# Performance work log

Hardware: AMD Instinct MI355X
Metric: run time of the kernel (lower is better)

## Reference

```python
import jax, jax.numpy as jnp
import numpy as np

EMBED_DIM = 1024
NUM_HEADS = 16
HEAD_DIM = EMBED_DIM // NUM_HEADS
BATCH = 1
SEQ = 4096


def setup_inputs() -> dict:
    key = jax.random.key(0)
    ks = jax.random.split(key, 9)
    s = 1.0 / np.sqrt(EMBED_DIM)
    inp = {
        "x": jax.random.normal(ks[0], (BATCH, SEQ, EMBED_DIM), dtype=jnp.float32),
        "Wq": jax.random.uniform(ks[1], (EMBED_DIM, EMBED_DIM), jnp.float32, -s, s),
        "bq": jax.random.uniform(ks[2], (EMBED_DIM,), jnp.float32, -s, s),
        "Wk": jax.random.uniform(ks[3], (EMBED_DIM, EMBED_DIM), jnp.float32, -s, s),
        "bk": jax.random.uniform(ks[4], (EMBED_DIM,), jnp.float32, -s, s),
        "Wv": jax.random.uniform(ks[5], (EMBED_DIM, EMBED_DIM), jnp.float32, -s, s),
        "bv": jax.random.uniform(ks[6], (EMBED_DIM,), jnp.float32, -s, s),
        "Wo": jax.random.uniform(ks[7], (EMBED_DIM, EMBED_DIM), jnp.float32, -s, s),
        "bo": jax.random.uniform(ks[8], (EMBED_DIM,), jnp.float32, -s, s),
    }
    return inp


def _attention(x, Wq, bq, Wk, bk, Wv, bv, Wo, bo):
    B, S, E = x.shape
    # project and split heads: [B, H, S, D]
    def split_heads(t):
        return t.reshape(B, S, NUM_HEADS, HEAD_DIM).transpose(0, 2, 1, 3)
    q = split_heads(x @ Wq + bq)
    k = split_heads(x @ Wk + bk)
    v = split_heads(x @ Wv + bv)
    scale = 1.0 / np.sqrt(HEAD_DIM).astype(np.float32)
    # scores: [B, H, S, S] (torch code materializes these per query chunk;
    # math is identical computed in one shot)
    scores = jnp.einsum("bhqd,bhkd->bhqk", q, k) * scale
    attn = jax.nn.softmax(scores, axis=-1)  # dropout p=0 -> identity
    out = jnp.einsum("bhqk,bhkd->bhqd", attn, v)
    out = out.transpose(0, 2, 1, 3).reshape(B, S, E)
    return out @ Wo + bo


def reference(x, Wq, bq, Wk, bk, Wv, bv, Wo, bo):
    return _attention(x, Wq, bq, Wk, bk, Wv, bv, Wo, bo)
```

## Files before the change

### kernel.cpp

```cpp
#include <hip/hip_runtime.h>
#include <stdint.h>

typedef __bf16 bf16;
typedef __bf16 bf16x2 __attribute__((ext_vector_type(2)));
typedef __bf16 bf16x8 __attribute__((ext_vector_type(8)));
typedef float f32x4 __attribute__((ext_vector_type(4)));
typedef float f32x16 __attribute__((ext_vector_type(16)));
typedef uint32_t u32x2 __attribute__((ext_vector_type(2)));

#define EMB 1024
#define SEQ 4096
#define NH 16
#define HD 64

__device__ __forceinline__ void glds16(const void* g, void* l) {
    __builtin_amdgcn_global_load_lds(
        (const __attribute__((address_space(1))) uint32_t*)(uintptr_t)g,
        (__attribute__((address_space(3))) uint32_t*)(uintptr_t)l,
        16, 0, 0);
}

union PU { bf16x2 h; uint32_t u; };
__device__ __forceinline__ uint32_t pack_bf16(float a, float b) {
    PU p; p.h = (bf16x2){(bf16)a, (bf16)b}; return p.u;
}
union FU { bf16x8 v; uint32_t u[4]; };

template<int NT>
__device__ __forceinline__ void transpose_tile(const float* in, bf16* out,
                                               int R, int C, int rbase, int cbase,
                                               bf16* tile ) {
    const int t = threadIdx.x;
    constexpr int PASSES = 512 / NT;
#pragma unroll
    for (int p = 0; p < PASSES; ++p) {
        int idx = t + p * NT;
        int r = idx >> 3;
        int seg = idx & 7;
        const float* src = in + (size_t)(rbase + r) * C + cbase + seg * 8;
        f32x4 a = *(const f32x4*)src;
        f32x4 b = *(const f32x4*)(src + 4);
#pragma unroll
        for (int i = 0; i < 4; ++i) {
            tile[r * 81 + seg * 8 + i]     = (bf16)a[i];
            tile[r * 81 + seg * 8 + 4 + i] = (bf16)b[i];
        }
    }
    __syncthreads();
#pragma unroll
    for (int p = 0; p < PASSES; ++p) {
        int idx = t + p * NT;
        int r = idx >> 3;
        int seg = idx & 7;
        bf16x8 v;
#pragma unroll
        for (int i = 0; i < 8; ++i) v[i] = tile[(seg * 8 + i) * 81 + r];
        *(bf16x8*)(out + (size_t)(cbase + r) * R + rbase + seg * 8) = v;
    }
}

__global__ __launch_bounds__(256) void prep_k(const float* __restrict__ W0,
                                              const float* __restrict__ W1,
                                              const float* __restrict__ W2,
                                              bf16* __restrict__ o0,
                                              bf16* __restrict__ o1,
                                              bf16* __restrict__ o2,
                                              const float* __restrict__ x,
                                              bf16* __restrict__ xb) {
    __shared__ bf16 tile[64 * 81];
    if (blockIdx.z < 3) {
        const float* in = blockIdx.z == 0 ? W0 : (blockIdx.z == 1 ? W1 : W2);
        bf16* out = blockIdx.z == 0 ? o0 : (blockIdx.z == 1 ? o1 : o2);
        transpose_tile<256>(in, out, EMB, EMB, blockIdx.y * 64, blockIdx.x * 64, tile);
    } else {
        size_t linear = blockIdx.y * 16 + blockIdx.x;
#pragma unroll
        for (int i = 0; i < 4; ++i) {
            size_t base = linear * 16384 + (size_t)i * 4096 + threadIdx.x * 16;
#pragma unroll
            for (int h = 0; h < 2; ++h) {
                f32x4 a = *(const f32x4*)(x + base + h * 8);
                f32x4 b = *(const f32x4*)(x + base + h * 8 + 4);
                bf16x8 v;
#pragma unroll
                for (int j = 0; j < 4; ++j) { v[j] = (bf16)a[j]; v[4 + j] = (bf16)b[j]; }
                *(bf16x8*)(xb + base + h * 8) = v;
            }
        }
    }
}

__global__ __launch_bounds__(256) void transpose_k(const float* __restrict__ in,
                                                   bf16* __restrict__ out,
                                                   int R, int C) {
    __shared__ bf16 tile[64 * 81];
    transpose_tile<256>(in, out, R, C, blockIdx.y * 64, blockIdx.x * 64, tile);
}

template<bool A_BF16, bool FUSED>
__global__ __launch_bounds__(256, 3) void gemm_m97(
    const void* __restrict__ A,
    const bf16* __restrict__ Wt0, const bf16* __restrict__ Wt1,
    const bf16* __restrict__ Wt2,
    const float* __restrict__ b0, const float* __restrict__ b1,
    const float* __restrict__ b2,
    void* __restrict__ out0, void* __restrict__ out1,
    bf16* __restrict__ outVt) {
    constexpr int SMEM_BYTES = A_BF16 ? (FUSED ? 18432 : 16384) : 24576;
    __shared__ __align__(16) uint8_t smem[SMEM_BYTES];
    float* aF = (float*)smem;
    bf16*  aB = (bf16*)smem;
    bf16*  bL = (bf16*)(smem + (A_BF16 ? 8192 : 16384));

    const int t = threadIdx.x;
    const int lane = t & 63;
    const int wave = t >> 6;
    const int l15 = lane & 15;
    const int quad = lane >> 4;
    const int wrow = (wave >> 1) * 64;
    const int wcol = (wave & 1) * 64;
    const int nb = blockIdx.x;
    const int which = FUSED ? (nb >> 3) : 0;
    const int ncol = (FUSED ? (nb & 7) : nb) * 128;
    const int mblock = blockIdx.y * 128;

    const bf16* Wt = FUSED ? (which == 0 ? Wt0 : (which == 1 ? Wt1 : Wt2)) : Wt0;
    const float* bias = FUSED ? (which == 0 ? b0 : (which == 1 ? b1 : b2)) : b0;

    float bv[4];
#pragma unroll
    for (int nt = 0; nt < 4; ++nt) bv[nt] = bias[ncol + wcol + nt * 16 + l15];

    f32x4 acc[4][4];
#pragma unroll
    for (int mt = 0; mt < 4; ++mt)
#pragma unroll
        for (int nt = 0; nt < 4; ++nt) acc[mt][nt] = (f32x4){0.f, 0.f, 0.f, 0.f};

    const int a4row = lane >> 3, a4seg = lane & 7;
    const int b2row = lane >> 2, b2seg = lane & 3;

    for (int k0 = 0; k0 < EMB; k0 += 32) {
        __syncthreads();
        if constexpr (!A_BF16) {
#pragma unroll
            for (int i = 0; i < 4; ++i) {
                int row = i * 32 + wave * 8 + a4row;
                int sg = a4seg ^ (row & 7);
                glds16((const float*)A + (size_t)(mblock + row) * EMB + k0 + sg * 4,
                       smem + i * 4096 + wave * 1024);
            }
        } else {
#pragma unroll
            for (int i = 0; i < 2; ++i) {
                int row = i * 64 + wave * 16 + b2row;
                int sg = b2seg ^ ((row >> 1) & 3);
                glds16((const bf16*)A + (size_t)(mblock + row) * EMB + k0 + sg * 8,
                       smem + i * 4096 + wave * 1024);
            }
        }
#pragma unroll
        for (int i = 0; i < 2; ++i) {
            int row = i * 64 + wave * 16 + b2row;
            int sg = b2seg ^ ((row >> 1) & 3);
            glds16(Wt + (size_t)(ncol + row) * EMB + k0 + sg * 8,
                   (uint8_t*)bL + i * 4096 + wave * 1024);
        }
        __syncthreads();

        bf16x8 af[4], bfr[4];
#pragma unroll
        for (int mt = 0; mt < 4; ++mt) {
            int rl = wrow + mt * 16 + l15;
            if constexpr (!A_BF16) {
                f32x4 lo = *(const f32x4*)(aF + rl * 32 + ((2 * quad)     ^ (rl & 7)) * 4);
                f32x4 hi = *(const f32x4*)(aF + rl * 32 + ((2 * quad + 1) ^ (rl & 7)) * 4);
#pragma unroll
                for (int j = 0; j < 4; ++j) {
                    af[mt][j]     = (bf16)lo[j];
                    af[mt][4 + j] = (bf16)hi[j];
                }
            } else {
                af[mt] = *(const bf16x8*)(aB + rl * 32 + (quad ^ ((rl >> 1) & 3)) * 8);
            }
        }
#pragma unroll
        for (int nt = 0; nt < 4; ++nt) {
            int rl = wcol + nt * 16 + l15;
            bfr[nt] = *(const bf16x8*)(bL + rl * 32 + (quad ^ ((rl >> 1) & 3)) * 8);
        }
#pragma unroll
        for (int mt = 0; mt < 4; ++mt)
#pragma unroll
            for (int nt = 0; nt < 4; ++nt)
                acc[mt][nt] = __builtin_amdgcn_mfma_f32_16x16x32_bf16(
                    af[mt], bfr[nt], acc[mt][nt], 0, 0, 0);
    }

    if (!FUSED || which < 2) {
        void* outp = FUSED ? (which == 0 ? out0 : out1) : out0;
#pragma unroll
        for (int mt = 0; mt < 4; ++mt)
#pragma unroll
            for (int nt = 0; nt < 4; ++nt)
#pragma unroll
                for (int r = 0; r < 4; ++r) {
                    size_t row = mblock + wrow + mt * 16 + quad * 4 + r;
                    size_t col = ncol + wcol + nt * 16 + l15;
                    float v = acc[mt][nt][r] + bv[nt];
                    if constexpr (FUSED) ((bf16*)outp)[row * EMB + col] = (bf16)v;
                    else                 ((float*)outp)[row * EMB + col] = v;
                }
    } else if constexpr (FUSED) {
        __syncthreads();
        bf16* tr = (bf16*)smem + wave * 2304;
#pragma unroll
        for (int ch = 0; ch < 2; ++ch) {
#pragma unroll
            for (int mt = 0; mt < 4; ++mt)
#pragma unroll
                for (int ntl = 0; ntl < 2; ++ntl)
#pragma unroll
                    for (int r = 0; r < 4; ++r) {
                        int d_local = ntl * 16 + l15;
                        int s_local = mt * 16 + quad * 4 + r;
                        int nt = 2 * ch + ntl;
                        tr[d_local * 72 + s_local] = (bf16)(acc[mt][nt][r] + bv[nt]);
                    }
            int d2 = lane & 31, h2 = lane >> 5;
#pragma unroll
            for (int j = 0; j < 4; ++j) {
                bf16x8 v = *(const bf16x8*)(tr + d2 * 72 + h2 * 32 + j * 8);
                *(bf16x8*)(outVt + (size_t)(ncol + wcol + ch * 32 + d2) * SEQ +
                           mblock + wrow + h2 * 32 + j * 8) = v;
            }
        }
    }
}

__global__ __launch_bounds__(256, 2) void attn_k(bf16* __restrict__ QO,
                                                 const bf16* __restrict__ Km,
                                                 const bf16* __restrict__ Vt,
                                                 const float* __restrict__ Wo,
                                                 bf16* __restrict__ wt_o) {
    __shared__ bf16 k_lds[2][64 * 64];
    __shared__ bf16 v_lds[2][64 * 64];

    const int t = threadIdx.x;
    const int lane = t & 63;
    const int wave = t >> 6;
    const int l31 = lane & 31;
    const int hi = lane >> 5;
    const int l7 = lane & 7;
    const int head = blockIdx.y;
    const int qbase = blockIdx.x * 128 + wave * 32;
    const float QSCALE = 0.125f * 1.4426950408889634f;

    const int srow = wave * 16 + (lane >> 3);
    const int ssg  = lane & 7;

    bf16x8 qf[4];
#pragma unroll
    for (int s = 0; s < 4; ++s) {
        bf16x8 raw = *(const bf16x8*)(QO + (size_t)(qbase + l31) * EMB +
                                      head * HD + s * 16 + hi * 8);
#pragma unroll
        for (int j = 0; j < 8; ++j) qf[s][j] = (bf16)((float)raw[j] * QSCALE);
    }

    f32x16 o_acc[2];
#pragma unroll
    for (int db = 0; db < 2; ++db)
#pragma unroll
        for (int z = 0; z < 16; ++z) o_acc[db][z] = 0.f;
    float l_run = 0.f;

#define STAGE(buf, kbv)                                                               \
    do {                                                                              \
        _Pragma("unroll")                                                             \
        for (int i = 0; i < 2; ++i) {                                                 \
            int rr = srow + i * 8;                                                    \
            int sg = ssg ^ (rr & 7);                                                  \
            glds16(Km + (size_t)((kbv) + rr) * EMB + head * HD + sg * 8,              \
                   &k_lds[buf][(wave * 16 + i * 8) * 64]);                            \
            glds16(Vt + (size_t)(head * HD + rr) * SEQ + (kbv) + sg * 8,              \
                   &v_lds[buf][(wave * 16 + i * 8) * 64]);                            \
        }                                                                             \
    } while (0)

#define COMPUTE(buf)                                                                  \
    do {                                                                              \
        f32x16 sa[2];                                                                 \
        _Pragma("unroll")                                                             \
        for (int b = 0; b < 2; ++b)                                                   \
            _Pragma("unroll")                                                         \
            for (int z = 0; z < 16; ++z) sa[b][z] = 0.f;                              \
        __builtin_amdgcn_s_setprio(1);                                                \
        _Pragma("unroll")                                                             \
        for (int s = 0; s < 4; ++s) {                                                 \
            bf16x8 kf0 = *(const bf16x8*)&k_lds[buf][(l31) * 64 +                     \
                            (((2 * s + hi) ^ l7) * 8)];                               \
            bf16x8 kf1 = *(const bf16x8*)&k_lds[buf][(32 + l31) * 64 +                \
                            (((2 * s + hi) ^ l7) * 8)];                               \
            sa[0] = __builtin_amdgcn_mfma_f32_32x32x16_bf16(kf0, qf[s], sa[0], 0, 0, 0);\
            sa[1] = __builtin_amdgcn_mfma_f32_32x32x16_bf16(kf1, qf[s], sa[1], 0, 0, 0);\
        }                                                                             \
        __builtin_amdgcn_s_setprio(0);                                                \
        uint32_t u0[2][4], u1[2][4];                                                  \
        _Pragma("unroll")                                                             \
        for (int b = 0; b < 2; ++b)                                                   \
            _Pragma("unroll")                                                         \
            for (int i = 0; i < 4; ++i) {                                             \
                float p0 = __builtin_amdgcn_exp2f(sa[b][4 * i + 0]);                  \
                float p1 = __builtin_amdgcn_exp2f(sa[b][4 * i + 1]);                  \
                float p2 = __builtin_amdgcn_exp2f(sa[b][4 * i + 2]);                  \
                float p3 = __builtin_amdgcn_exp2f(sa[b][4 * i + 3]);                  \
                l_run += (p0 + p1) + (p2 + p3);                                       \
                u0[b][i] = pack_bf16(p0, p1);                                         \
                u1[b][i] = pack_bf16(p2, p3);                                         \
            }                                                                         \
        __builtin_amdgcn_s_setprio(1);                                                \
        _Pragma("unroll")                                                             \
        for (int tt = 0; tt < 4; ++tt) {                                              \
            const int b = tt >> 1, sp = tt & 1;                                       \
            u32x2 ra = __builtin_amdgcn_permlane32_swap(                              \
                u0[b][2 * sp], u0[b][2 * sp + 1], false, false);                      \
            u32x2 rb = __builtin_amdgcn_permlane32_swap(                              \
                u1[b][2 * sp], u1[b][2 * sp + 1], false, false);                      \
            FU A;                                                                     \
            A.u[0] = ra[0]; A.u[1] = rb[0]; A.u[2] = ra[1]; A.u[3] = rb[1];           \
            bf16x8 vf0 = *(const bf16x8*)&v_lds[buf][(l31) * 64 +                     \
                            (((2 * tt + hi) ^ l7) * 8)];                              \
            bf16x8 vf1 = *(const bf16x8*)&v_lds[buf][(32 + l31) * 64 +                \
                            (((2 * tt + hi) ^ l7) * 8)];                              \
            o_acc[0] = __builtin_amdgcn_mfma_f32_32x32x16_bf16(A.v, vf0, o_acc[0], 0, 0, 0);\
            o_acc[1] = __builtin_amdgcn_mfma_f32_32x32x16_bf16(A.v, vf1, o_acc[1], 0, 0, 0);\
        }                                                                             \
        __builtin_amdgcn_s_setprio(0);                                                \
    } while (0)

    STAGE(0, 0);
    for (int kb = 0; kb < SEQ; kb += 128) {
        __syncthreads();
        STAGE(1, kb + 64);
        COMPUTE(0);
        __syncthreads();
        if (kb + 128 < SEQ) STAGE(0, kb + 128);
        COMPUTE(1);
    }
#undef STAGE
#undef COMPUTE

    l_run += __shfl_xor(l_run, 32);
    float inv = 1.0f / l_run;
    float invr[16];
#pragma unroll
    for (int reg = 0; reg < 16; ++reg)
        invr[reg] = __shfl(inv, (reg & 3) + 8 * (reg >> 2) + 4 * hi);
#pragma unroll
    for (int db = 0; db < 2; ++db)
#pragma unroll
        for (int reg = 0; reg < 16; ++reg) {
            int q = (reg & 3) + 8 * (reg >> 2) + 4 * hi;
            QO[(size_t)(qbase + q) * EMB + head * HD + db * 32 + l31] =
                (bf16)(o_acc[db][reg] * invr[reg]);
        }

    if (Wo != nullptr) {
        int bid = blockIdx.y * gridDim.x + blockIdx.x;
        if (bid < 256) {
            __syncthreads();
            bf16* tile = &k_lds[0][0];
            int ty = bid >> 4, tx = bid & 15;
            transpose_tile<256>(Wo, wt_o, EMB, EMB, ty * 64, tx * 64, tile);
        }
    }
}

extern "C" void kernel_launch(void* const* d_in, const int* in_sizes, int n_in,
                              void* d_out, int out_size, void* d_ws, size_t ws_size,
                              hipStream_t stream) {
    const float* x  = (const float*)d_in[0];
    const float* Wq = (const float*)d_in[1];
    const float* bq = (const float*)d_in[2];
    const float* Wk = (const float*)d_in[3];
    const float* bk = (const float*)d_in[4];
    const float* Wv = (const float*)d_in[5];
    const float* bv = (const float*)d_in[6];
    const float* Wo = (const float*)d_in[7];
    const float* bo = (const float*)d_in[8];

    const size_t MAT = (size_t)SEQ * EMB;
    const size_t WMT = (size_t)EMB * EMB;

    bf16* o16   = (bf16*)d_out;
    bf16* Wt_q  = o16;
    bf16* Wt_k  = o16 + WMT;
    bf16* Wt_v  = o16 + 2 * WMT;
    bf16* Vtb   = o16 + 3 * WMT;

    bf16* wsb   = (bf16*)d_ws;
    bf16* QOb   = wsb;
    bf16* Kb    = wsb + MAT;
    bf16* xb    = wsb + 2 * MAT;

    dim3 blk(256);
    dim3 gP(16, 16, 4);
    dim3 gF(24, SEQ / 128);
    dim3 gO(EMB / 128, SEQ / 128);

    if (ws_size >= 3 * MAT * sizeof(bf16)) {
        prep_k<<<gP, blk, 0, stream>>>(Wq, Wk, Wv, Wt_q, Wt_k, Wt_v, x, xb);

        gemm_m97<true, true><<<gF, blk, 0, stream>>>(
            xb, Wt_q, Wt_k, Wt_v, bq, bk, bv, QOb, Kb, Vtb);

        dim3 gA(SEQ / 128, NH);
        attn_k<<<gA, blk, 0, stream>>>(QOb, Kb, Vtb, Wo, xb);

        gemm_m97<true, false><<<gO, blk, 0, stream>>>(
            QOb, xb, nullptr, nullptr, bo, nullptr, nullptr, d_out, nullptr, nullptr);
    } else {
        bf16* Wt_o = wsb + MAT;
        dim3 gTW(EMB / 64, EMB / 64);
        transpose_k<<<gTW, blk, 0, stream>>>(Wq, Wt_q, EMB, EMB);
        transpose_k<<<gTW, blk, 0, stream>>>(Wk, Wt_k, EMB, EMB);
        transpose_k<<<gTW, blk, 0, stream>>>(Wv, Wt_v, EMB, EMB);
        gemm_m97<false, true><<<gF, blk, 0, stream>>>(
            x, Wt_q, Wt_k, Wt_v, bq, bk, bv, QOb, Kb, Vtb);
        dim3 gA(SEQ / 128, NH);
        attn_k<<<gA, blk, 0, stream>>>(QOb, Kb, Vtb, nullptr, nullptr);
        transpose_k<<<gTW, blk, 0, stream>>>(Wo, Wt_o, EMB, EMB);
        gemm_m97<true, false><<<gO, blk, 0, stream>>>(
            QOb, Wt_o, nullptr, nullptr, bo, nullptr, nullptr, d_out, nullptr, nullptr);
    }
}
```

Baseline: 228.2 us.

## Split key tiles across wave pairs with LDS reduction of partial outputs

New measurement: 223.0 us. 2.3% less time.

```diff
diff --git a/kernel.cpp b/kernel.cpp
--- a/kernel.cpp
+++ b/kernel.cpp
@@ -25,6 +25,7 @@
     PU p; p.h = (bf16x2){(bf16)a, (bf16)b}; return p.u;
 }
 union FU { bf16x8 v; uint32_t u[4]; };
+union OU { f32x16 v; f32x4 q4[4]; };
 
 template<int NT>
 __device__ __forceinline__ void transpose_tile(const float* in, bf16* out,
@@ -243,8 +244,7 @@
                                                  const bf16* __restrict__ Vt,
                                                  const float* __restrict__ Wo,
                                                  bf16* __restrict__ wt_o) {
-    __shared__ bf16 k_lds[2][64 * 64];
-    __shared__ bf16 v_lds[2][64 * 64];
+    __shared__ __align__(16) bf16 kv_lds[4][64 * 64];
 
     const int t = threadIdx.x;
     const int lane = t & 63;
@@ -253,27 +253,29 @@
     const int hi = lane >> 5;
     const int l7 = lane & 7;
     const int head = blockIdx.y;
-    const int qbase = blockIdx.x * 128 + wave * 32;
+    const int qh = wave >> 1;
+    const int kb = wave & 1;
+    const int qbase = blockIdx.x * 128 + qh * 64;
     const float QSCALE = 0.125f * 1.4426950408889634f;
 
     const int srow = wave * 16 + (lane >> 3);
     const int ssg  = lane & 7;
 
-    bf16x8 qf[4];
-#pragma unroll
-    for (int s = 0; s < 4; ++s) {
-        bf16x8 raw = *(const bf16x8*)(QO + (size_t)(qbase + l31) * EMB +
-                                      head * HD + s * 16 + hi * 8);
-#pragma unroll
-        for (int j = 0; j < 8; ++j) qf[s][j] = (bf16)((float)raw[j] * QSCALE);
-    }
-
-    f32x16 o_acc[2];
-#pragma unroll
-    for (int db = 0; db < 2; ++db)
-#pragma unroll
-        for (int z = 0; z < 16; ++z) o_acc[db][z] = 0.f;
-    float l_run = 0.f;
+    bf16x8 qf[2][4];
+#pragma unroll
+    for (int qg = 0; qg < 2; ++qg)
+#pragma unroll
+        for (int s = 0; s < 4; ++s) {
+            bf16x8 raw = *(const bf16x8*)(QO + (size_t)(qbase + qg * 32 + l31) * EMB +
+                                          head * HD + s * 16 + hi * 8);
+#pragma unroll
+            for (int j = 0; j < 8; ++j) qf[qg][s][j] = (bf16)((float)raw[j] * QSCALE);
+        }
+
+    f32x16 o00, o01, o10, o11;
+#pragma unroll
+    for (int z = 0; z < 16; ++z) { o00[z] = 0.f; o01[z] = 0.f; o10[z] = 0.f; o11[z] = 0.f; }
+    float l0 = 0.f, l1 = 0.f;
 
 #define STAGE(buf, kbv)                                                               \
     do {                                                                              \
@@ -282,95 +284,134 @@
             int rr = srow + i * 8;                                                    \
             int sg = ssg ^ (rr & 7);                                                  \
             glds16(Km + (size_t)((kbv) + rr) * EMB + head * HD + sg * 8,              \
-                   &k_lds[buf][(wave * 16 + i * 8) * 64]);                            \
+                   &kv_lds[buf][(wave * 16 + i * 8) * 64]);                           \
             glds16(Vt + (size_t)(head * HD + rr) * SEQ + (kbv) + sg * 8,              \
-                   &v_lds[buf][(wave * 16 + i * 8) * 64]);                            \
+                   &kv_lds[2 + (buf)][(wave * 16 + i * 8) * 64]);                     \
         }                                                                             \
     } while (0)
 
 #define COMPUTE(buf)                                                                  \
     do {                                                                              \
-        f32x16 sa[2];                                                                 \
+        f32x16 sa0, sa1;                                                              \
         _Pragma("unroll")                                                             \
-        for (int b = 0; b < 2; ++b)                                                   \
-            _Pragma("unroll")                                                         \
-            for (int z = 0; z < 16; ++z) sa[b][z] = 0.f;                              \
-        __builtin_amdgcn_s_setprio(1);                                                \
+        for (int z = 0; z < 16; ++z) { sa0[z] = 0.f; sa1[z] = 0.f; }                  \
         _Pragma("unroll")                                                             \
         for (int s = 0; s < 4; ++s) {                                                 \
-            bf16x8 kf0 = *(const bf16x8*)&k_lds[buf][(l31) * 64 +                     \
+            bf16x8 kf = *(const bf16x8*)&kv_lds[buf][(kb * 32 + l31) * 64 +           \
                             (((2 * s + hi) ^ l7) * 8)];                               \
-            bf16x8 kf1 = *(const bf16x8*)&k_lds[buf][(32 + l31) * 64 +                \
-                            (((2 * s + hi) ^ l7) * 8)];                               \
-            sa[0] = __builtin_amdgcn_mfma_f32_32x32x16_bf16(kf0, qf[s], sa[0], 0, 0, 0);\
-            sa[1] = __builtin_amdgcn_mfma_f32_32x32x16_bf16(kf1, qf[s], sa[1], 0, 0, 0);\
+            sa0 = __builtin_amdgcn_mfma_f32_32x32x16_bf16(kf, qf[0][s], sa0, 0, 0, 0);\
+            sa1 = __builtin_amdgcn_mfma_f32_32x32x16_bf16(kf, qf[1][s], sa1, 0, 0, 0);\
         }                                                                             \
-        __builtin_amdgcn_s_setprio(0);                                                \
-        uint32_t u0[2][4], u1[2][4];                                                  \
+        uint32_t u00[4], u01[4], u10[4], u11[4];                                      \
         _Pragma("unroll")                                                             \
-        for (int b = 0; b < 2; ++b)                                                   \
-            _Pragma("unroll")                                                         \
-            for (int i = 0; i < 4; ++i) {                                             \
-                float p0 = __builtin_amdgcn_exp2f(sa[b][4 * i + 0]);                  \
-                float p1 = __builtin_amdgcn_exp2f(sa[b][4 * i + 1]);                  \
-                float p2 = __builtin_amdgcn_exp2f(sa[b][4 * i + 2]);                  \
-                float p3 = __builtin_amdgcn_exp2f(sa[b][4 * i + 3]);                  \
-                l_run += (p0 + p1) + (p2 + p3);                                       \
-                u0[b][i] = pack_bf16(p0, p1);                                         \
-                u1[b][i] = pack_bf16(p2, p3);                                         \
+        for (int i = 0; i < 4; ++i) {                                                 \
+            float a0 = __builtin_amdgcn_exp2f(sa0[4 * i + 0]);                        \
+            float a1 = __builtin_amdgcn_exp2f(sa0[4 * i + 1]);                        \
+            float a2 = __builtin_amdgcn_exp2f(sa0[4 * i + 2]);                        \
+            float a3 = __builtin_amdgcn_exp2f(sa0[4 * i + 3]);                        \
+            l0 += (a0 + a1) + (a2 + a3);                                              \
+            u00[i] = pack_bf16(a0, a1);                                               \
+            u01[i] = pack_bf16(a2, a3);                                               \
+            float b0 = __builtin_amdgcn_exp2f(sa1[4 * i + 0]);                        \
+            float b1 = __builtin_amdgcn_exp2f(sa1[4 * i + 1]);                        \
+            float b2 = __builtin_amdgcn_exp2f(sa1[4 * i + 2]);                        \
+            float b3 = __builtin_amdgcn_exp2f(sa1[4 * i + 3]);                        \
+            l1 += (b0 + b1) + (b2 + b3);                                              \
+            u10[i] = pack_bf16(b0, b1);                                               \
+            u11[i] = pack_bf16(b2, b3);                                               \
+        }                                                                             \
+        _Pragma("unroll")                                                             \
+        for (int sp = 0; sp < 2; ++sp) {                                              \
+            const int tt = kb * 2 + sp;                                               \
+            FU A0, A1;                                                                \
+            {                                                                         \
+                u32x2 ra = __builtin_amdgcn_permlane32_swap(u00[2 * sp], u00[2 * sp + 1], false, false); \
+                u32x2 rb = __builtin_amdgcn_permlane32_swap(u01[2 * sp], u01[2 * sp + 1], false, false); \
+                A0.u[0] = ra[0]; A0.u[1] = rb[0]; A0.u[2] = ra[1]; A0.u[3] = rb[1];   \
             }                                                                         \
-        __builtin_amdgcn_s_setprio(1);                                                \
-        _Pragma("unroll")                                                             \
-        for (int tt = 0; tt < 4; ++tt) {                                              \
-            const int b = tt >> 1, sp = tt & 1;                                       \
-            u32x2 ra = __builtin_amdgcn_permlane32_swap(                              \
-                u0[b][2 * sp], u0[b][2 * sp + 1], false, false);                      \
-            u32x2 rb = __builtin_amdgcn_permlane32_swap(                              \
-                u1[b][2 * sp], u1[b][2 * sp + 1], false, false);                      \
-            FU A;                                                                     \
-            A.u[0] = ra[0]; A.u[1] = rb[0]; A.u[2] = ra[1]; A.u[3] = rb[1];           \
-            bf16x8 vf0 = *(const bf16x8*)&v_lds[buf][(l31) * 64 +                     \
+            {                                                                         \
+                u32x2 ra = __builtin_amdgcn_permlane32_swap(u10[2 * sp], u10[2 * sp + 1], false, false); \
+                u32x2 rb = __builtin_amdgcn_permlane32_swap(u11[2 * sp], u11[2 * sp + 1], false, false); \
+                A1.u[0] = ra[0]; A1.u[1] = rb[0]; A1.u[2] = ra[1]; A1.u[3] = rb[1];   \
+            }                                                                         \
+            bf16x8 vf0 = *(const bf16x8*)&kv_lds[2 + (buf)][(l31) * 64 +              \
                             (((2 * tt + hi) ^ l7) * 8)];                              \
-            bf16x8 vf1 = *(const bf16x8*)&v_lds[buf][(32 + l31) * 64 +                \
+            bf16x8 vf1 = *(const bf16x8*)&kv_lds[2 + (buf)][(32 + l31) * 64 +         \
                             (((2 * tt + hi) ^ l7) * 8)];                              \
-            o_acc[0] = __builtin_amdgcn_mfma_f32_32x32x16_bf16(A.v, vf0, o_acc[0], 0, 0, 0);\
-            o_acc[1] = __builtin_amdgcn_mfma_f32_32x32x16_bf16(A.v, vf1, o_acc[1], 0, 0, 0);\
+            o00 = __builtin_amdgcn_mfma_f32_32x32x16_bf16(A0.v, vf0, o00, 0, 0, 0);   \
+            o01 = __builtin_amdgcn_mfma_f32_32x32x16_bf16(A0.v, vf1, o01, 0, 0, 0);   \
+            o10 = __builtin_amdgcn_mfma_f32_32x32x16_bf16(A1.v, vf0, o10, 0, 0, 0);   \
+            o11 = __builtin_amdgcn_mfma_f32_32x32x16_bf16(A1.v, vf1, o11, 0, 0, 0);   \
         }                                                                             \
-        __builtin_amdgcn_s_setprio(0);                                                \
     } while (0)
 
     STAGE(0, 0);
-    for (int kb = 0; kb < SEQ; kb += 128) {
+    for (int kb2 = 0; kb2 < SEQ; kb2 += 128) {
         __syncthreads();
-        STAGE(1, kb + 64);
+        STAGE(1, kb2 + 64);
         COMPUTE(0);
         __syncthreads();
-        if (kb + 128 < SEQ) STAGE(0, kb + 128);
+        if (kb2 + 128 < SEQ) STAGE(0, kb2 + 128);
         COMPUTE(1);
     }
 #undef STAGE
 #undef COMPUTE
 
-    l_run += __shfl_xor(l_run, 32);
-    float inv = 1.0f / l_run;
-    float invr[16];
-#pragma unroll
-    for (int reg = 0; reg < 16; ++reg)
-        invr[reg] = __shfl(inv, (reg & 3) + 8 * (reg >> 2) + 4 * hi);
-#pragma unroll
-    for (int db = 0; db < 2; ++db)
+    float* red = (float*)&kv_lds[0][0];
+    __syncthreads();
+    if (kb == 1) {
+        red[qh * 128 + lane] = l0;
+        red[qh * 128 + 64 + lane] = l1;
+    }
+    __syncthreads();
+    if (kb == 0) {
+        l0 += red[qh * 128 + lane];
+        l1 += red[qh * 128 + 64 + lane];
+    }
+    __syncthreads();
+    if (kb == 1) {
+        OU w0, w1, w2, w3;
+        w0.v = o00; w1.v = o01; w2.v = o10; w3.v = o11;
+#pragma unroll
+        for (int j = 0; j < 4; ++j) {
+            *(f32x4*)&red[qh * 4096 + (0 * 64 + lane) * 16 + j * 4] = w0.q4[j];
+            *(f32x4*)&red[qh * 4096 + (1 * 64 + lane) * 16 + j * 4] = w1.q4[j];
+            *(f32x4*)&red[qh * 4096 + (2 * 64 + lane) * 16 + j * 4] = w2.q4[j];
+            *(f32x4*)&red[qh * 4096 + (3 * 64 + lane) * 16 + j * 4] = w3.q4[j];
+        }
+    }
+    __syncthreads();
+    if (kb == 0) {
+        OU w0, w1, w2, w3;
+        w0.v = o00; w1.v = o01; w2.v = o10; w3.v = o11;
+#pragma unroll
+        for (int j = 0; j < 4; ++j) {
+            w0.q4[j] += *(const f32x4*)&red[qh * 4096 + (0 * 64 + lane) * 16 + j * 4];
+            w1.q4[j] += *(const f32x4*)&red[qh * 4096 + (1 * 64 + lane) * 16 + j * 4];
+            w2.q4[j] += *(const f32x4*)&red[qh * 4096 + (2 * 64 + lane) * 16 + j * 4];
+            w3.q4[j] += *(const f32x4*)&red[qh * 4096 + (3 * 64 + lane) * 16 + j * 4];
+        }
+        l0 += __shfl_xor(l0, 32);
+        l1 += __shfl_xor(l1, 32);
+        float inv0 = 1.0f / l0;
+        float inv1 = 1.0f / l1;
 #pragma unroll
         for (int reg = 0; reg < 16; ++reg) {
             int q = (reg & 3) + 8 * (reg >> 2) + 4 * hi;
-            QO[(size_t)(qbase + q) * EMB + head * HD + db * 32 + l31] =
-                (bf16)(o_acc[db][reg] * invr[reg]);
-        }
+            float i0 = __shfl(inv0, q);
+            float i1 = __shfl(inv1, q);
+            QO[(size_t)(qbase + q) * EMB + head * HD + l31]      = (bf16)(w0.v[reg] * i0);
+            QO[(size_t)(qbase + q) * EMB + head * HD + 32 + l31] = (bf16)(w1.v[reg] * i0);
+            QO[(size_t)(qbase + 32 + q) * EMB + head * HD + l31]      = (bf16)(w2.v[reg] * i1);
+            QO[(size_t)(qbase + 32 + q) * EMB + head * HD + 32 + l31] = (bf16)(w3.v[reg] * i1);
+        }
+    }
+    __syncthreads();
 
     if (Wo != nullptr) {
         int bid = blockIdx.y * gridDim.x + blockIdx.x;
         if (bid < 256) {
-            __syncthreads();
-            bf16* tile = &k_lds[0][0];
+            bf16* tile = &kv_lds[0][0];
             int ty = bid >> 4, tx = bid & 15;
             transpose_tile<256>(Wo, wt_o, EMB, EMB, ty * 64, tx * 64, tile);
         }
```
